# Performance work log

Measured on AMD Instinct MI355X. Metric: run time of the kernel, lower is better.

Reference implementation:

```python
import jax, jax.numpy as jnp
import numpy as np


def setup_inputs() -> dict:
    key = jax.random.key(0)
    k1, k2, k3 = jax.random.split(key, 3)
    B, N, E, A = 1024, 64, 64, 32
    emb_inputs = jax.random.normal(k1, (B, N, E), dtype=jnp.float32)
    W1 = jax.random.normal(k2, (E, A), dtype=jnp.float32) * (1.0 / np.sqrt(E))
    b1 = jnp.zeros((A,), dtype=jnp.float32)
    W2 = jax.random.normal(k3, (A, 1), dtype=jnp.float32) * (1.0 / np.sqrt(A))
    b2 = jnp.zeros((1,), dtype=jnp.float32)
    return {"emb_inputs": emb_inputs, "W1": W1, "b1": b1, "W2": W2, "b2": b2,
            "num_fields": N}


def reference(emb_inputs, W1, b1, W2, b2, num_fields):
    # Pairwise interaction indices (i < j), same order as torch double loop
    rowidx, colidx = np.triu_indices(num_fields, k=1)
    rowidx = jnp.asarray(rowidx)
    colidx = jnp.asarray(colidx)
    # inner: (B, NC2, E) elementwise product of field pairs
    inner = emb_inputs[:, rowidx] * emb_inputs[:, colidx]
    # tiny attention MLP: E -> A -> 1, softmax over the pair dim
    h = jax.nn.relu(jnp.einsum('bpe,ea->bpa', inner, W1) + b1)
    logits = jnp.einsum('bpa,ao->bpo', h, W2) + b2          # (B, NC2, 1)
    attn_scores = jax.nn.softmax(logits, axis=1)            # (B, NC2, 1)
    # dropout layers are identity in eval mode
    outputs = jnp.sum(inner * attn_scores, axis=1)          # (B, E)
    return outputs, attn_scores
```

## Files before the change

### kernel.cpp

```cpp
#include <hip/hip_runtime.h>

#define BATCH   1024
#define NF      64
#define EDIM    64
#define ADIM    32
#define NPAIR   2016
#define XSTR    72

typedef _Float16 f16;
typedef f16   f16x4  __attribute__((ext_vector_type(4)));
typedef f16   f16x8  __attribute__((ext_vector_type(8)));
typedef float f32x4  __attribute__((ext_vector_type(4)));
typedef float f32x16 __attribute__((ext_vector_type(16)));

__device__ __forceinline__ f16x8 asH(int4 v) {
    union { int4 i; f16x8 h; } u; u.i = v; return u.h;
}

__global__ __launch_bounds__(256, 4) void afm_kernel(
    const float* __restrict__ emb,
    const float* __restrict__ W1,
    const float* __restrict__ b1,
    const float* __restrict__ W2,
    const float* __restrict__ b2,
    float* __restrict__ out_vec,
    float* __restrict__ out_attn)
{
    __shared__ __align__(16) f16 xs[NF * XSTR];
    __shared__ __align__(16) f16 Xt[EDIM * XSTR];
    __shared__ __align__(16) f16 As[NF * XSTR];
    __shared__ float logits[NPAIR];
    __shared__ float red[8];
    __shared__ float partial[4][EDIM];

    const int t    = threadIdx.x;
    const int b    = blockIdx.x;
    const int wid  = t >> 6;
    const int lane = t & 63;
    const int g    = lane >> 4;
    const int m16  = lane & 15;
    const int h    = lane >> 5;
    const int l32  = lane & 31;
    const int l16  = lane & 15;
    const int hb   = l32 >> 4;

    const float4* xg4 = (const float4*)(emb + (size_t)b * NF * EDIM);
    #pragma unroll
    for (int it = 0; it < 4; ++it) {
        int idx = t + it * 256;
        int f = idx >> 4, e4 = (idx & 15) * 4;
        float4 v = xg4[idx];
        f16x4 pk = {(f16)v.x, (f16)v.y, (f16)v.z, (f16)v.w};
        *(f16x4*)&xs[f * XSTR + e4] = pk;
    }

    f16x8 w1a[4];
    #pragma unroll
    for (int q = 0; q < 4; ++q)
        #pragma unroll
        for (int jj = 0; jj < 8; ++jj)
            w1a[q][jj] = (f16)W1[(16 * q + 8 * h + jj) * ADIM + l32];

    float b1v[16], w2v[16];
    #pragma unroll
    for (int r = 0; r < 16; ++r) {
        int a = (r & 3) + 8 * (r >> 2) + 4 * h;
        b1v[r] = b1[a];
        w2v[r] = W2[a];
    }
    const float b2s = b2[0];
    __syncthreads();

    {
        const unsigned short* xsu = (const unsigned short*)xs;
        #pragma unroll
        for (int it = 0; it < 2; ++it) {
            int cid = t + it * 256;
            int e = cid & 63, c = cid >> 6;
            unsigned int d[4];
            #pragma unroll
            for (int r2 = 0; r2 < 4; ++r2) {
                unsigned lo = xsu[(8 * c + 2 * r2)     * XSTR + e];
                unsigned hi = xsu[(8 * c + 2 * r2 + 1) * XSTR + e];
                d[r2] = lo | (hi << 16);
            }
            int4 w4 = {(int)d[0], (int)d[1], (int)d[2], (int)d[3]};
            *(int4*)&Xt[e * XSTR + 8 * c] = w4;
        }
    }
    __syncthreads();

    int probe = __builtin_amdgcn_mov_dpp(l16, 0x124, 0xF, 0xF, false);
    const bool plus4 = (probe == ((l16 + 4) & 15));
    const int  s0r   = plus4 ? (wid + 1) : (wid + 5);

    int4 xi4[4], xj4[4];

    auto LOADX = [&](int row, int4* d) {
        #pragma unroll
        for (int q = 0; q < 4; ++q)
            d[q] = *(const int4*)&xs[row * XSTR + 16 * q + 8 * h];
    };
    auto ROT4D = [&](int4* d, int& jv) {
        #pragma unroll
        for (int q = 0; q < 4; ++q) {
            d[q].x = __builtin_amdgcn_mov_dpp(d[q].x, 0x124, 0xF, 0xF, false);
            d[q].y = __builtin_amdgcn_mov_dpp(d[q].y, 0x124, 0xF, 0xF, false);
            d[q].z = __builtin_amdgcn_mov_dpp(d[q].z, 0x124, 0xF, 0xF, false);
            d[q].w = __builtin_amdgcn_mov_dpp(d[q].w, 0x124, 0xF, 0xF, false);
        }
        jv = __builtin_amdgcn_mov_dpp(jv, 0x124, 0xF, 0xF, false);
    };
    auto SUB = [&](const int4* xa, const int4* xb, int iv, int jv) {
        f32x16 acc = {};
        #pragma unroll
        for (int q = 0; q < 4; ++q) {
            f16x8 prod = asH(xa[q]) * asH(xb[q]);
            acc = __builtin_amdgcn_mfma_f32_32x32x16_f16(w1a[q], prod, acc, 0, 0, 0);
        }
        float t0 = 0.f, t1 = 0.f;
        #pragma unroll
        for (int r = 0; r < 16; r += 2) {
            t0 += fmaxf(acc[r]     + b1v[r],     0.f) * w2v[r];
            t1 += fmaxf(acc[r + 1] + b1v[r + 1], 0.f) * w2v[r + 1];
        }
        float tr = t0 + t1;
        tr += __shfl_xor(tr, 32);
        int imin = min(iv, jv), jmax = max(iv, jv);
        int p = ((imin * (127 - imin)) >> 1) + jmax - imin - 1;
        if (lane < 32) logits[p] = tr + b2s;
    };

    LOADX(l32, xi4);
    {
        int jv = 32 + 16 * hb + ((l16 + wid) & 15);
        LOADX(jv, xj4);
        #pragma unroll
        for (int k = 0; k < 4; ++k) {
            SUB(xi4, xj4, l32, jv);
            if (k < 3) ROT4D(xj4, jv);
        }
    }
    {
        int jv = 32 + 16 * (1 - hb) + ((l16 + wid) & 15);
        LOADX(jv, xj4);
        #pragma unroll
        for (int k = 0; k < 4; ++k) {
            SUB(xi4, xj4, l32, jv);
            if (k < 3) ROT4D(xj4, jv);
        }
    }
    {
        int jv = 16 * hb + ((l16 + s0r) & 15);
        LOADX(jv, xj4);
        SUB(xi4, xj4, l32, jv);
        ROT4D(xj4, jv);
        SUB(xi4, xj4, l32, jv);
    }
    {
        int jv = 16 + ((l16 + wid + 8 * hb) & 15);
        LOADX(l16, xi4);
        LOADX(jv, xj4);
        SUB(xi4, xj4, l16, jv);
        ROT4D(xj4, jv);
        SUB(xi4, xj4, l16, jv);
    }
    {
        int jv = 32 + 16 * hb + ((l16 + s0r) & 15);
        LOADX(32 + l32, xi4);
        LOADX(jv, xj4);
        SUB(xi4, xj4, 32 + l32, jv);
        ROT4D(xj4, jv);
        SUB(xi4, xj4, 32 + l32, jv);
    }
    {
        int jv = 48 + ((l16 + wid + 8 * hb) & 15);
        LOADX(32 + l16, xi4);
        LOADX(jv, xj4);
        SUB(xi4, xj4, 32 + l16, jv);
        ROT4D(xj4, jv);
        SUB(xi4, xj4, 32 + l16, jv);
    }
    __syncthreads();

    float lv[8];
    #pragma unroll
    for (int k = 0; k < 8; ++k) {
        int p = t + 256 * k;
        lv[k] = (p < NPAIR) ? logits[p] : -INFINITY;
    }
    float m = lv[0];
    #pragma unroll
    for (int k = 1; k < 8; ++k) m = fmaxf(m, lv[k]);
    #pragma unroll
    for (int off = 32; off; off >>= 1) m = fmaxf(m, __shfl_xor(m, off));
    if (lane == 0) red[wid] = m;
    __syncthreads();
    if (t == 0) red[4] = fmaxf(fmaxf(red[0], red[1]), fmaxf(red[2], red[3]));
    __syncthreads();
    m = red[4];

    float s = 0.0f;
    #pragma unroll
    for (int k = 0; k < 8; ++k) {
        float ev = __expf(lv[k] - m);
        lv[k] = ev;
        s += ev;
    }
    #pragma unroll
    for (int off = 32; off; off >>= 1) s += __shfl_xor(s, off);
    __syncthreads();
    if (lane == 0) red[wid] = s;
    __syncthreads();
    if (t == 0) red[5] = red[0] + red[1] + red[2] + red[3];
    __syncthreads();
    const float inv = 1.0f / red[5];

    #pragma unroll
    for (int k = 0; k < 8; ++k) {
        int p = t + 256 * k;
        if (p < NPAIR) {
            float av = lv[k] * inv;
            out_attn[(size_t)b * NPAIR + p] = av;
            int i = (int)(63.5f - 0.5f * sqrtf(16129.0f - 8.0f * (float)p));
            int Ti = (i * (127 - i)) >> 1;
            if (p < Ti)      { --i; Ti = (i * (127 - i)) >> 1; }
            else { int Tn = ((i + 1) * (126 - i)) >> 1; if (p >= Tn) { ++i; Ti = Tn; } }
            int j = p - Ti + i + 1;
            f16 ah = (f16)av;
            As[i * XSTR + j] = ah;
            As[j * XSTR + i] = ah;
        }
    }
    if (t < NF) As[t * XSTR + t] = (f16)0.f;
    __syncthreads();

    const int itile = wid;
    f32x4 yacc[4];
    #pragma unroll
    for (int et = 0; et < 4; ++et) yacc[et] = (f32x4){0.f, 0.f, 0.f, 0.f};

    const f16* arow = &As[(itile * 16 + m16) * XSTR];
    f16x8 af0 = *(const f16x8*)(arow + 8 * g);
    f16x8 af1 = *(const f16x8*)(arow + 32 + 8 * g);
    #pragma unroll
    for (int et = 0; et < 4; ++et) {
        const f16* xtr = &Xt[(et * 16 + m16) * XSTR];
        f16x8 bf0 = *(const f16x8*)(xtr + 8 * g);
        f16x8 bf1 = *(const f16x8*)(xtr + 32 + 8 * g);
        yacc[et] = __builtin_amdgcn_mfma_f32_16x16x32_f16(af0, bf0, yacc[et], 0, 0, 0);
        yacc[et] = __builtin_amdgcn_mfma_f32_16x16x32_f16(af1, bf1, yacc[et], 0, 0, 0);
    }

    #pragma unroll
    for (int et = 0; et < 4; ++et) {
        float v = 0.f;
        #pragma unroll
        for (int r = 0; r < 4; ++r) {
            int i = itile * 16 + 4 * g + r;
            int e = et * 16 + m16;
            v = fmaf((float)xs[i * XSTR + e], yacc[et][r], v);
        }
        v += __shfl_xor(v, 16);
        v += __shfl_xor(v, 32);
        if (g == 0) partial[wid][et * 16 + m16] = v;
    }
    __syncthreads();
    if (t < EDIM)
        out_vec[(size_t)b * EDIM + t] = 0.5f *
            (partial[0][t] + partial[1][t] + partial[2][t] + partial[3][t]);
}

extern "C" void kernel_launch(void* const* d_in, const int* in_sizes, int n_in,
                              void* d_out, int out_size, void* d_ws, size_t ws_size,
                              hipStream_t stream) {
    const float* emb = (const float*)d_in[0];
    const float* W1  = (const float*)d_in[1];
    const float* b1  = (const float*)d_in[2];
    const float* W2  = (const float*)d_in[3];
    const float* b2  = (const float*)d_in[4];
    float* out_vec  = (float*)d_out;
    float* out_attn = (float*)d_out + (size_t)BATCH * EDIM;

    afm_kernel<<<BATCH, 256, 0, stream>>>(emb, W1, b1, W2, b2, out_vec, out_attn);
}
```

Baseline: 26.48 us.

## Alias softmax buffers in LDS, fuse softmax reductions, pack ReLU epilogue math

Logits, the attention matrix and the partial-sum buffer now share one LDS union buffer. This cuts shared memory per block, which could let more blocks stay resident, at the cost of an extra barrier before the space is reused. The max and sum reductions are merged into a single barrier pass that rescales per-wave sums with exp corrections, removing several __syncthreads. The ReLU/W2 epilogue is written with float2 vectors so it can map to packed FP32 instructions. The attention matrix row stride changes to 68, and its fragment loads are split into 8-byte pieces.

```diff
diff --git a/kernel.cpp b/kernel.cpp
--- a/kernel.cpp
+++ b/kernel.cpp
@@ -6,10 +6,12 @@
 #define ADIM    32
 #define NPAIR   2016
 #define XSTR    72
+#define ASTR    68
 
 typedef _Float16 f16;
 typedef f16   f16x4  __attribute__((ext_vector_type(4)));
 typedef f16   f16x8  __attribute__((ext_vector_type(8)));
+typedef float f32x2  __attribute__((ext_vector_type(2)));
 typedef float f32x4  __attribute__((ext_vector_type(4)));
 typedef float f32x16 __attribute__((ext_vector_type(16)));
 
@@ -28,10 +30,11 @@
 {
     __shared__ __align__(16) f16 xs[NF * XSTR];
     __shared__ __align__(16) f16 Xt[EDIM * XSTR];
-    __shared__ __align__(16) f16 As[NF * XSTR];
-    __shared__ float logits[NPAIR];
+    __shared__ __align__(16) char Ubuf[9088];
+    float* logits = (float*)Ubuf;
+    float (*partial)[EDIM] = (float (*)[EDIM])(Ubuf + 8064);
+    f16* As = (f16*)Ubuf;
     __shared__ float red[8];
-    __shared__ float partial[4][EDIM];
 
     const int t    = threadIdx.x;
     const int b    = blockIdx.x;
@@ -61,12 +64,13 @@
         for (int jj = 0; jj < 8; ++jj)
             w1a[q][jj] = (f16)W1[(16 * q + 8 * h + jj) * ADIM + l32];
 
-    float b1v[16], w2v[16];
-    #pragma unroll
-    for (int r = 0; r < 16; ++r) {
+    f32x2 b1f2[8], w2f2[8];
+    #pragma unroll
+    for (int rr = 0; rr < 8; ++rr) {
+        int r = 2 * rr;
         int a = (r & 3) + 8 * (r >> 2) + 4 * h;
-        b1v[r] = b1[a];
-        w2v[r] = W2[a];
+        b1f2[rr] = (f32x2){b1[a], b1[a + 1]};
+        w2f2[rr] = (f32x2){W2[a], W2[a + 1]};
     }
     const float b2s = b2[0];
     __syncthreads();
@@ -118,13 +122,14 @@
             f16x8 prod = asH(xa[q]) * asH(xb[q]);
             acc = __builtin_amdgcn_mfma_f32_32x32x16_f16(w1a[q], prod, acc, 0, 0, 0);
         }
-        float t0 = 0.f, t1 = 0.f;
-        #pragma unroll
-        for (int r = 0; r < 16; r += 2) {
-            t0 += fmaxf(acc[r]     + b1v[r],     0.f) * w2v[r];
-            t1 += fmaxf(acc[r + 1] + b1v[r + 1], 0.f) * w2v[r + 1];
-        }
-        float tr = t0 + t1;
+        f32x2 tr2 = {0.f, 0.f};
+        #pragma unroll
+        for (int rr = 0; rr < 8; ++rr) {
+            f32x2 a2 = {acc[2 * rr], acc[2 * rr + 1]};
+            f32x2 h2 = __builtin_elementwise_max(a2 + b1f2[rr], (f32x2){0.f, 0.f});
+            tr2 += h2 * w2f2[rr];
+        }
+        float tr = tr2.x + tr2.y;
         tr += __shfl_xor(tr, 32);
         int imin = min(iv, jv), jmax = max(iv, jv);
         int p = ((imin * (127 - imin)) >> 1) + jmax - imin - 1;
@@ -189,38 +194,33 @@
         int p = t + 256 * k;
         lv[k] = (p < NPAIR) ? logits[p] : -INFINITY;
     }
-    float m = lv[0];
-    #pragma unroll
-    for (int k = 1; k < 8; ++k) m = fmaxf(m, lv[k]);
-    #pragma unroll
-    for (int off = 32; off; off >>= 1) m = fmaxf(m, __shfl_xor(m, off));
-    if (lane == 0) red[wid] = m;
-    __syncthreads();
-    if (t == 0) red[4] = fmaxf(fmaxf(red[0], red[1]), fmaxf(red[2], red[3]));
-    __syncthreads();
-    m = red[4];
-
-    float s = 0.0f;
+    float mw = lv[0];
+    #pragma unroll
+    for (int k = 1; k < 8; ++k) mw = fmaxf(mw, lv[k]);
+    #pragma unroll
+    for (int off = 32; off; off >>= 1) mw = fmaxf(mw, __shfl_xor(mw, off));
+
+    float sw = 0.0f;
     #pragma unroll
     for (int k = 0; k < 8; ++k) {
-        float ev = __expf(lv[k] - m);
+        float ev = __expf(lv[k] - mw);
         lv[k] = ev;
-        s += ev;
-    }
-    #pragma unroll
-    for (int off = 32; off; off >>= 1) s += __shfl_xor(s, off);
-    __syncthreads();
-    if (lane == 0) red[wid] = s;
-    __syncthreads();
-    if (t == 0) red[5] = red[0] + red[1] + red[2] + red[3];
-    __syncthreads();
-    const float inv = 1.0f / red[5];
+        sw += ev;
+    }
+    #pragma unroll
+    for (int off = 32; off; off >>= 1) sw += __shfl_xor(sw, off);
+    if (lane == 0) { red[wid] = mw; red[4 + wid] = sw; }
+    __syncthreads();
+    const float mg = fmaxf(fmaxf(red[0], red[1]), fmaxf(red[2], red[3]));
+    const float ssum = red[4] * __expf(red[0] - mg) + red[5] * __expf(red[1] - mg)
+                     + red[6] * __expf(red[2] - mg) + red[7] * __expf(red[3] - mg);
+    const float fsc = __expf(mw - mg) / ssum;
 
     #pragma unroll
     for (int k = 0; k < 8; ++k) {
         int p = t + 256 * k;
         if (p < NPAIR) {
-            float av = lv[k] * inv;
+            float av = lv[k] * fsc;
             out_attn[(size_t)b * NPAIR + p] = av;
             int i = (int)(63.5f - 0.5f * sqrtf(16129.0f - 8.0f * (float)p));
             int Ti = (i * (127 - i)) >> 1;
@@ -228,21 +228,30 @@
             else { int Tn = ((i + 1) * (126 - i)) >> 1; if (p >= Tn) { ++i; Ti = Tn; } }
             int j = p - Ti + i + 1;
             f16 ah = (f16)av;
-            As[i * XSTR + j] = ah;
-            As[j * XSTR + i] = ah;
-        }
-    }
-    if (t < NF) As[t * XSTR + t] = (f16)0.f;
+            As[i * ASTR + j] = ah;
+            As[j * ASTR + i] = ah;
+        }
+    }
+    if (t < NF) As[t * ASTR + t] = (f16)0.f;
     __syncthreads();
 
     const int itile = wid;
+    const f16* arow = &As[(itile * 16 + m16) * ASTR];
+    f16x4 afa0 = *(const f16x4*)(arow + 8 * g);
+    f16x4 afb0 = *(const f16x4*)(arow + 8 * g + 4);
+    f16x4 afa1 = *(const f16x4*)(arow + 32 + 8 * g);
+    f16x4 afb1 = *(const f16x4*)(arow + 32 + 8 * g + 4);
+    __syncthreads();
+    f16x8 af0, af1;
+    #pragma unroll
+    for (int j = 0; j < 4; ++j) {
+        af0[j] = afa0[j]; af0[4 + j] = afb0[j];
+        af1[j] = afa1[j]; af1[4 + j] = afb1[j];
+    }
+
     f32x4 yacc[4];
     #pragma unroll
     for (int et = 0; et < 4; ++et) yacc[et] = (f32x4){0.f, 0.f, 0.f, 0.f};
-
-    const f16* arow = &As[(itile * 16 + m16) * XSTR];
-    f16x8 af0 = *(const f16x8*)(arow + 8 * g);
-    f16x8 af1 = *(const f16x8*)(arow + 32 + 8 * g);
     #pragma unroll
     for (int et = 0; et < 4; ++et) {
         const f16* xtr = &Xt[(et * 16 + m16) * XSTR];
```

Result: no change. 26.28 us (-0.8%).
